# Kernel optimization log

Hardware: AMD Instinct MI355X
Metric: run time of the kernel (lower is better)

## Reference

```python
import jax, jax.numpy as jnp
import numpy as np

NUM_LAYERS = 5  # shared parameters across layers


def _crelu(z):
    # complex ReLU: ReLU applied independently to real and imag parts
    return jnp.maximum(z.real, 0.0) + 1j * jnp.maximum(z.imag, 0.0)


def _layer(Habs2, diagH, noise, maxpow, v, ar, dl, rc):
    # ---- u step ----
    # cov: [B,K,1] = |H|^2 @ |v|^2 (sum over last dim keepdim is identity for width-1) + noise
    cov = jnp.sum(Habs2 @ (jnp.abs(v) ** 2), axis=-1, keepdims=True) + noise[..., None]
    u = diagH[..., None] * v / cov  # [B,K,1] complex
    # ---- w step ---- (w_poly=None branch)
    err = 1.0 - jnp.conj(u) * diagH[..., None] * v
    w = 1.0 / err  # [B,K,1] complex
    # ---- v step ----
    v_tilde = jnp.conj(diagH)[..., None] * u * w  # [B,K,1]
    ul = (jnp.abs(u) ** 2) * jnp.abs(w)  # real [B,K,1]
    ul = jnp.sum(jnp.abs(jnp.swapaxes(Habs2, -2, -1) @ ul), axis=-1, keepdims=True)
    mu = jnp.maximum(jnp.abs(v_tilde) / jnp.sqrt(maxpow)[..., None] - ul, 0.0)
    ula = (ul + mu).astype(v_tilde.dtype)
    # ar + diagload branches: [B,K,1,1] @ [1,C] -> [B,K,1,C]
    vt = (v_tilde / ula)[..., None] @ ar + v_tilde[..., None] @ dl
    # nonlin + recombination: [B,K,1,C] @ [C,1] -> [B,K,1,1]
    vt = _crelu(vt) @ rc
    v_new = vt[..., 0]  # [B,K,1]
    # power correction
    cur = jnp.maximum(maxpow[..., None], jnp.abs(v_new) ** 2)
    corr = jnp.minimum(jnp.sqrt(maxpow[..., None] / cur), 1.0)
    return v_new * corr, u, w


def setup_inputs() -> dict:
    key = jax.random.key(0)
    ks = jax.random.split(key, 12)
    B, K, C = 64, 512, 4
    s = 1.0 / np.sqrt(C + 1)
    inp = {
        "h_re": jax.random.normal(ks[0], (B, K, K), jnp.float32),
        "h_im": jax.random.normal(ks[1], (B, K, K), jnp.float32),
        "user_noise_pow": jax.random.uniform(ks[2], (B, K), jnp.float32, 0.1, 1.0),
        "bss_maxpow": jnp.ones((B, K), jnp.float32),
        "v_in_re": jax.random.normal(ks[3], (B, K, 1), jnp.float32) * 0.5,
        "v_in_im": jax.random.normal(ks[4], (B, K, 1), jnp.float32) * 0.5,
        "ar_re": jax.random.normal(ks[5], (1, C), jnp.float32) * s,
        "ar_im": jax.random.normal(ks[6], (1, C), jnp.float32) * s,
        "dl_re": jax.random.normal(ks[7], (1, C), jnp.float32) * s,
        "dl_im": jax.random.normal(ks[8], (1, C), jnp.float32) * s,
        "rc_re": jax.random.normal(ks[9], (C, 1), jnp.float32) * s,
        "rc_im": jax.random.normal(ks[10], (C, 1), jnp.float32) * s,
    }
    return inp


def reference(h_re, h_im, user_noise_pow, bss_maxpow, v_in_re, v_in_im,
              ar_re, ar_im, dl_re, dl_im, rc_re, rc_im):
    H = (h_re + 1j * h_im).astype(jnp.complex64)
    Habs2 = h_re * h_re + h_im * h_im  # |H|^2, real [B,K,K]
    diagH = jnp.diagonal(H, axis1=-2, axis2=-1)  # [B,K]
    v = (v_in_re + 1j * v_in_im).astype(jnp.complex64)
    ar = (ar_re + 1j * ar_im).astype(jnp.complex64)
    dl = (dl_re + 1j * dl_im).astype(jnp.complex64)
    rc = (rc_re + 1j * rc_im).astype(jnp.complex64)
    vs = []
    for _ in range(NUM_LAYERS):
        v, u, w = _layer(Habs2, diagH, user_noise_pow, bss_maxpow, v, ar, dl, rc)
        vs.append(v)
    vstack = jnp.stack(vs, 0)  # [L,B,K,1] complex
    # return real/imag stacked so the output is a real tensor: [L,B,K,1,2]
    return jnp.stack([vstack.real, vstack.imag], axis=-1)
```

## Files before the change

kernel.cpp:

```cpp
#include <hip/hip_runtime.h>

#define B    64
#define K    512
#define C    4
#define NL   5
#define BK   (B*K)
#define ROWS 128
#define NT   1024
#define GRID (B*4)

typedef _Float16 half_t;
typedef _Float16 half8 __attribute__((ext_vector_type(8)));
typedef float    f4    __attribute__((ext_vector_type(4)));

#define HABS_BYTES (ROWS*K*2)
#define VST_OFF    (HABS_BYTES)
#define PART_OFF   (VST_OFF + K*8)
#define XSQ_OFF    (PART_OFF + 8*K*4)
#define DAB_OFF    (XSQ_OFF + K*4)
#define MPL_OFF    (DAB_OFF + ROWS*4)
#define NZ_OFF     (MPL_OFF + K*4)
#define SMEM_BYTES (NZ_OFF + ROWS*4)

__device__ __forceinline__ float ld_l3(const float* p) {
    return __uint_as_float(__hip_atomic_load((const unsigned*)p,
        __ATOMIC_RELAXED, __HIP_MEMORY_SCOPE_AGENT));
}
__device__ __forceinline__ void st_l3(float* p, float v) {
    __hip_atomic_store((unsigned*)p, __float_as_uint(v),
        __ATOMIC_RELAXED, __HIP_MEMORY_SCOPE_AGENT);
}
__device__ __forceinline__ void st_l3_2(float2* p, float2 v) {
    unsigned long long u = ((unsigned long long)__float_as_uint(v.y) << 32)
                         | (unsigned long long)__float_as_uint(v.x);
    __hip_atomic_store((unsigned long long*)p, u,
        __ATOMIC_RELAXED, __HIP_MEMORY_SCOPE_AGENT);
}
__device__ __forceinline__ float2 ld_l3_2(const float2* p) {
    unsigned long long u = __hip_atomic_load((const unsigned long long*)p,
        __ATOMIC_RELAXED, __HIP_MEMORY_SCOPE_AGENT);
    return make_float2(__uint_as_float((unsigned)(u & 0xffffffffu)),
                       __uint_as_float((unsigned)(u >> 32)));
}

__device__ __forceinline__ void quartet_barrier(unsigned* qb, unsigned target) {
    __syncthreads();
    if (threadIdx.x == 0) {
        __hip_atomic_fetch_add(qb, 1u, __ATOMIC_RELAXED,
                               __HIP_MEMORY_SCOPE_AGENT);
        while (__hip_atomic_load(qb, __ATOMIC_RELAXED,
                                 __HIP_MEMORY_SCOPE_AGENT) < target)
            __builtin_amdgcn_s_sleep(4);
    }
    __syncthreads();
}

__global__ __launch_bounds__(NT, 4) void k_all(
    const float* __restrict__ hre,  const float* __restrict__ him,
    const float* __restrict__ noise,const float* __restrict__ mp,
    const float* __restrict__ vre,  const float* __restrict__ vim,
    const float* __restrict__ ar_re,const float* __restrict__ ar_im,
    const float* __restrict__ dl_re,const float* __restrict__ dl_im,
    const float* __restrict__ rc_re,const float* __restrict__ rc_im,
    float2* __restrict__ vtilde,
    float*  __restrict__ ulpart,
    unsigned* __restrict__ bar,
    float* __restrict__ out)
{
    extern __shared__ char smem[];
    half_t* habs = (half_t*)smem;
    float2* vst  = (float2*)(smem + VST_OFF);
    float*  part = (float*) (smem + PART_OFF);
    float*  xsq  = (float*) (smem + XSQ_OFF);
    float*  dab  = (float*) (smem + DAB_OFF);
    float*  mpl  = (float*) (smem + MPL_OFF);
    float*  nz   = (float*) (smem + NZ_OFF);

    const int tid  = threadIdx.x;
    const int lane = tid & 63;
    const int w    = tid >> 6;
    const int b    = blockIdx.x & 63;
    const int q    = blockIdx.x >> 6;
    const int j0   = q * ROWS;
    unsigned* qb   = bar + ((unsigned)b << 5);

    {
        const size_t gb = ((size_t)b * K + j0) * K;
        const f4* rp = (const f4*)(hre + gb);
        const f4* ip = (const f4*)(him + gb);
        f4 lr0[2], lr1[2], li0[2], li1[2];
        lr0[0] = __builtin_nontemporal_load(rp + tid * 2);
        lr1[0] = __builtin_nontemporal_load(rp + tid * 2 + 1);
        li0[0] = __builtin_nontemporal_load(ip + tid * 2);
        li1[0] = __builtin_nontemporal_load(ip + tid * 2 + 1);
#pragma unroll
        for (int i = 0; i < 8; ++i) {
            const int cur = i & 1, nxt = cur ^ 1;
            if (i < 7) {
                const int e4 = (i + 1) * (NT * 2) + tid * 2;
                lr0[nxt] = __builtin_nontemporal_load(rp + e4);
                lr1[nxt] = __builtin_nontemporal_load(rp + e4 + 1);
                li0[nxt] = __builtin_nontemporal_load(ip + e4);
                li1[nxt] = __builtin_nontemporal_load(ip + e4 + 1);
            }
            const f4 r0 = lr0[cur], r1 = lr1[cur];
            const f4 m0 = li0[cur], m1 = li1[cur];
            float s[8];
            s[0] = r0.x*r0.x + m0.x*m0.x; s[1] = r0.y*r0.y + m0.y*m0.y;
            s[2] = r0.z*r0.z + m0.z*m0.z; s[3] = r0.w*r0.w + m0.w*m0.w;
            s[4] = r1.x*r1.x + m1.x*m1.x; s[5] = r1.y*r1.y + m1.y*m1.y;
            s[6] = r1.z*r1.z + m1.z*m1.z; s[7] = r1.w*r1.w + m1.w*m1.w;
            half8 hh;
#pragma unroll
            for (int t = 0; t < 8; ++t) hh[t] = (_Float16)s[t];
            const int e = i * (NT * 8) + tid * 8;
            *(half8*)(habs + e) = hh;
            const int row  = e >> 9;
            const int col0 = e & (K - 1);
            const int j    = j0 + row;
            if (j >= col0 && j < col0 + 8) dab[row] = s[j - col0];
        }
        if (tid < K) {
            float a = vre[b * K + tid], c = vim[b * K + tid];
            vst[tid] = make_float2(a, c);
            xsq[tid] = a * a + c * c;
            mpl[tid] = mp[b * K + tid];
        } else if (tid < K + ROWS) {
            nz[tid - K] = noise[b * K + j0 + (tid - K)];
        }
    }
    __syncthreads();

    for (int l = 0; l < NL; ++l) {
        const int buf = l & 1;
        const f4 xa = ((const f4*)xsq)[lane * 2];
        const f4 xb = ((const f4*)xsq)[lane * 2 + 1];
        half8 h[8];
        float rs[8];
#pragma unroll
        for (int r = 0; r < 8; ++r) {
            h[r] = *(const half8*)(habs + ((w * 8 + r) * K + lane * 8));
            float acc = (float)h[r][0]*xa.x + (float)h[r][1]*xa.y +
                        (float)h[r][2]*xa.z + (float)h[r][3]*xa.w +
                        (float)h[r][4]*xb.x + (float)h[r][5]*xb.y +
                        (float)h[r][6]*xb.z + (float)h[r][7]*xb.w;
#pragma unroll
            for (int off = 32; off; off >>= 1) acc += __shfl_xor(acc, off, 64);
            rs[r] = acc;
        }
        float ulv_own = 0.f;
        if (lane < 8) {
            const int row = w * 8 + lane;
            const int j   = j0 + row;
            const int bj  = b * K + j;
            float s = lane==0?rs[0]:lane==1?rs[1]:lane==2?rs[2]:lane==3?rs[3]:
                      lane==4?rs[4]:lane==5?rs[5]:lane==6?rs[6]:rs[7];
            const float cov = s + nz[row];
            const float d2  = dab[row];
            const float A   = d2 * xsq[j];
            const float ww  = cov / (cov - A);
            const float sc  = d2 * ww / cov;
            const float2 vv = vst[j];
            st_l3_2(&vtilde[buf * BK + bj], make_float2(sc * vv.x, sc * vv.y));
            ulv_own = A * ww / (cov * cov);
        }
        float ulv[8];
#pragma unroll
        for (int r = 0; r < 8; ++r) ulv[r] = __shfl(ulv_own, r, 64);

        float pw[8];
#pragma unroll
        for (int t = 0; t < 8; ++t) {
            pw[t] = (float)h[0][t]*ulv[0] + (float)h[1][t]*ulv[1] +
                    (float)h[2][t]*ulv[2] + (float)h[3][t]*ulv[3] +
                    (float)h[4][t]*ulv[4] + (float)h[5][t]*ulv[5] +
                    (float)h[6][t]*ulv[6] + (float)h[7][t]*ulv[7];
        }
        float* pr = part + (w & 7) * K + lane * 8;
        if (w < 8) {
#pragma unroll
            for (int t = 0; t < 8; ++t) pr[t] = pw[t];
        }
        __syncthreads();
        if (w >= 8) {
#pragma unroll
            for (int t = 0; t < 8; ++t) pr[t] += pw[t];
        }
        __syncthreads();
        float s2 = 0.f;
        if (tid < K) {
            s2 = part[tid]       + part[K + tid]   + part[2*K + tid] +
                 part[3*K + tid] + part[4*K + tid] + part[5*K + tid] +
                 part[6*K + tid] + part[7*K + tid];
            st_l3(&ulpart[(size_t)buf * (B*4*K) + ((size_t)(b*4 + q)) * K + tid],
                  s2);
        }
        quartet_barrier(qb, 4u * (unsigned)(l + 1));

        if (tid < K) {
            const int k  = tid;
            const int bk = b * K + k;
            const float* up = ulpart + (size_t)buf * (B*4*K) + (size_t)(b*4) * K;
            float ul = s2;
#pragma unroll
            for (int qq = 0; qq < 4; ++qq)
                if (qq != q) ul += ld_l3(up + qq * K + k);
            const float2 vt = ld_l3_2(&vtilde[buf * BK + bk]);
            const float p   = mpl[k];
            const float avt = sqrtf(vt.x*vt.x + vt.y*vt.y);
            const float mu  = fmaxf(avt / sqrtf(p) - ul, 0.f);
            const float inv = 1.f / (ul + mu);
            float ax = 0.f, ay = 0.f;
#pragma unroll
            for (int c = 0; c < C; ++c) {
                const float gre = ar_re[c] * inv + dl_re[c];
                const float gim = ar_im[c] * inv + dl_im[c];
                float zre = vt.x * gre - vt.y * gim;
                float zim = vt.x * gim + vt.y * gre;
                zre = fmaxf(zre, 0.f);
                zim = fmaxf(zim, 0.f);
                ax += zre * rc_re[c] - zim * rc_im[c];
                ay += zre * rc_im[c] + zim * rc_re[c];
            }
            const float n2   = ax*ax + ay*ay;
            const float cur  = fmaxf(p, n2);
            const float corr = fminf(sqrtf(p / cur), 1.f);
            ax *= corr; ay *= corr;
            if ((k >> 7) == q)
                ((float2*)out)[(size_t)l * BK + bk] = make_float2(ax, ay);
            vst[k] = make_float2(ax, ay);
            xsq[k] = ax * ax + ay * ay;
        }
        __syncthreads();
    }
}

extern "C" void kernel_launch(void* const* d_in, const int* in_sizes, int n_in,
                              void* d_out, int out_size, void* d_ws, size_t ws_size,
                              hipStream_t stream) {
    const float* hre   = (const float*)d_in[0];
    const float* him   = (const float*)d_in[1];
    const float* noise = (const float*)d_in[2];
    const float* mp    = (const float*)d_in[3];
    const float* vre   = (const float*)d_in[4];
    const float* vim   = (const float*)d_in[5];
    const float* ar_re = (const float*)d_in[6];
    const float* ar_im = (const float*)d_in[7];
    const float* dl_re = (const float*)d_in[8];
    const float* dl_im = (const float*)d_in[9];
    const float* rc_re = (const float*)d_in[10];
    const float* rc_im = (const float*)d_in[11];
    float* out = (float*)d_out;

    char*     ws     = (char*)d_ws;
    float2*   vtilde = (float2*)ws;
    float*    ulpart = (float*)(ws + 2*(size_t)BK*8);
    unsigned* bar    = (unsigned*)(ws + 2*(size_t)BK*8 + 2*(size_t)B*4*K*4);

    static bool attr_done = false;
    if (!attr_done) {
        hipFuncSetAttribute((const void*)k_all,
                            hipFuncAttributeMaxDynamicSharedMemorySize,
                            SMEM_BYTES);
        attr_done = true;
    }

    hipMemsetAsync(bar, 0, B * 32 * sizeof(unsigned), stream);

    hipLaunchKernelGGL(k_all, dim3(GRID), dim3(NT), SMEM_BYTES, stream,
                       hre, him, noise, mp, vre, vim,
                       ar_re, ar_im, dl_re, dl_im, rc_re, rc_im,
                       vtilde, ulpart, bar, out);
}
```

Measured before the change: 192.8 us.

## Keep |H|^2 tile in registers instead of shared memory across layers

The fp16 |H|^2 tile now stays in per-thread registers (8 half8 per thread) instead of a shared-memory buffer, and rows are interleaved across warps. The first layer's row sums are fused into the load loop. The partial-sum reduction now uses 16 shared slices with one barrier instead of two. The quartet barrier has every wave's lane 0 spin rather than using a trailing __syncthreads, and the vtilde load is hoisted. The aim is to remove LDS traffic and barriers, at the cost of higher register pressure and weaker memory-ordering guarantees on the spin wait.

```diff
diff --git a/kernel.cpp b/kernel.cpp
--- a/kernel.cpp
+++ b/kernel.cpp
@@ -13,14 +13,14 @@
 typedef _Float16 half8 __attribute__((ext_vector_type(8)));
 typedef float    f4    __attribute__((ext_vector_type(4)));
 
-#define HABS_BYTES (ROWS*K*2)
-#define VST_OFF    (HABS_BYTES)
-#define PART_OFF   (VST_OFF + K*8)
-#define XSQ_OFF    (PART_OFF + 8*K*4)
-#define DAB_OFF    (XSQ_OFF + K*4)
-#define MPL_OFF    (DAB_OFF + ROWS*4)
+#define PART_OFF   0
+#define VST_OFF    (36*K*4)
+#define XSQ_OFF    (VST_OFF + K*8)
+#define MPL_OFF    (XSQ_OFF + K*4)
 #define NZ_OFF     (MPL_OFF + K*4)
-#define SMEM_BYTES (NZ_OFF + ROWS*4)
+#define DAB_OFF    (NZ_OFF + ROWS*4)
+#define RSB_OFF    (DAB_OFF + ROWS*4)
+#define SMEM_BYTES (RSB_OFF + ROWS*4)
 
 __device__ __forceinline__ float ld_l3(const float* p) {
     return __uint_as_float(__hip_atomic_load((const unsigned*)p,
@@ -41,18 +41,6 @@
         __ATOMIC_RELAXED, __HIP_MEMORY_SCOPE_AGENT);
     return make_float2(__uint_as_float((unsigned)(u & 0xffffffffu)),
                        __uint_as_float((unsigned)(u >> 32)));
-}
-
-__device__ __forceinline__ void quartet_barrier(unsigned* qb, unsigned target) {
-    __syncthreads();
-    if (threadIdx.x == 0) {
-        __hip_atomic_fetch_add(qb, 1u, __ATOMIC_RELAXED,
-                               __HIP_MEMORY_SCOPE_AGENT);
-        while (__hip_atomic_load(qb, __ATOMIC_RELAXED,
-                                 __HIP_MEMORY_SCOPE_AGENT) < target)
-            __builtin_amdgcn_s_sleep(4);
-    }
-    __syncthreads();
 }
 
 __global__ __launch_bounds__(NT, 4) void k_all(
@@ -68,13 +56,13 @@
     float* __restrict__ out)
 {
     extern __shared__ char smem[];
-    half_t* habs = (half_t*)smem;
-    float2* vst  = (float2*)(smem + VST_OFF);
-    float*  part = (float*) (smem + PART_OFF);
-    float*  xsq  = (float*) (smem + XSQ_OFF);
-    float*  dab  = (float*) (smem + DAB_OFF);
-    float*  mpl  = (float*) (smem + MPL_OFF);
-    float*  nz   = (float*) (smem + NZ_OFF);
+    float*  part  = (float*) (smem + PART_OFF);
+    float2* vst   = (float2*)(smem + VST_OFF);
+    float*  xsq   = (float*) (smem + XSQ_OFF);
+    float*  mpl   = (float*) (smem + MPL_OFF);
+    float*  nz    = (float*) (smem + NZ_OFF);
+    float*  dab   = (float*) (smem + DAB_OFF);
+    float*  rsbuf = (float*) (smem + RSB_OFF);
 
     const int tid  = threadIdx.x;
     const int lane = tid & 63;
@@ -84,7 +72,20 @@
     const int j0   = q * ROWS;
     unsigned* qb   = bar + ((unsigned)b << 5);
 
+    if (tid < K) {
+        float a = vre[b * K + tid], c2 = vim[b * K + tid];
+        vst[tid] = make_float2(a, c2);
+        xsq[tid] = a * a + c2 * c2;
+        mpl[tid] = mp[b * K + tid];
+    } else if (tid < K + ROWS) {
+        nz[tid - K] = noise[b * K + j0 + (tid - K)];
+    }
+    __syncthreads();
+
+    half8 h[8];
     {
+        const f4 xa = ((const f4*)xsq)[lane * 2];
+        const f4 xb = ((const f4*)xsq)[lane * 2 + 1];
         const size_t gb = ((size_t)b * K + j0) * K;
         const f4* rp = (const f4*)(hre + gb);
         const f4* ip = (const f4*)(him + gb);
@@ -113,49 +114,41 @@
             half8 hh;
 #pragma unroll
             for (int t = 0; t < 8; ++t) hh[t] = (_Float16)s[t];
-            const int e = i * (NT * 8) + tid * 8;
-            *(half8*)(habs + e) = hh;
-            const int row  = e >> 9;
-            const int col0 = e & (K - 1);
+            h[i] = hh;
+            const int row  = i * 16 + w;
+            const int col0 = lane * 8;
             const int j    = j0 + row;
             if (j >= col0 && j < col0 + 8) dab[row] = s[j - col0];
-        }
-        if (tid < K) {
-            float a = vre[b * K + tid], c = vim[b * K + tid];
-            vst[tid] = make_float2(a, c);
-            xsq[tid] = a * a + c * c;
-            mpl[tid] = mp[b * K + tid];
-        } else if (tid < K + ROWS) {
-            nz[tid - K] = noise[b * K + j0 + (tid - K)];
-        }
-    }
-    __syncthreads();
+            float acc = s[0]*xa.x + s[1]*xa.y + s[2]*xa.z + s[3]*xa.w +
+                        s[4]*xb.x + s[5]*xb.y + s[6]*xb.z + s[7]*xb.w;
+#pragma unroll
+            for (int off = 32; off; off >>= 1) acc += __shfl_xor(acc, off, 64);
+            if (lane == 0) rsbuf[row] = acc;
+        }
+    }
 
     for (int l = 0; l < NL; ++l) {
         const int buf = l & 1;
-        const f4 xa = ((const f4*)xsq)[lane * 2];
-        const f4 xb = ((const f4*)xsq)[lane * 2 + 1];
-        half8 h[8];
-        float rs[8];
-#pragma unroll
-        for (int r = 0; r < 8; ++r) {
-            h[r] = *(const half8*)(habs + ((w * 8 + r) * K + lane * 8));
-            float acc = (float)h[r][0]*xa.x + (float)h[r][1]*xa.y +
-                        (float)h[r][2]*xa.z + (float)h[r][3]*xa.w +
-                        (float)h[r][4]*xb.x + (float)h[r][5]*xb.y +
-                        (float)h[r][6]*xb.z + (float)h[r][7]*xb.w;
-#pragma unroll
-            for (int off = 32; off; off >>= 1) acc += __shfl_xor(acc, off, 64);
-            rs[r] = acc;
+        if (l > 0) {
+            const f4 xa = ((const f4*)xsq)[lane * 2];
+            const f4 xb = ((const f4*)xsq)[lane * 2 + 1];
+#pragma unroll
+            for (int r = 0; r < 8; ++r) {
+                float acc = (float)h[r][0]*xa.x + (float)h[r][1]*xa.y +
+                            (float)h[r][2]*xa.z + (float)h[r][3]*xa.w +
+                            (float)h[r][4]*xb.x + (float)h[r][5]*xb.y +
+                            (float)h[r][6]*xb.z + (float)h[r][7]*xb.w;
+#pragma unroll
+                for (int off = 32; off; off >>= 1) acc += __shfl_xor(acc, off, 64);
+                if (lane == 0) rsbuf[r * 16 + w] = acc;
+            }
         }
         float ulv_own = 0.f;
         if (lane < 8) {
-            const int row = w * 8 + lane;
+            const int row = 16 * lane + w;
             const int j   = j0 + row;
             const int bj  = b * K + j;
-            float s = lane==0?rs[0]:lane==1?rs[1]:lane==2?rs[2]:lane==3?rs[3]:
-                      lane==4?rs[4]:lane==5?rs[5]:lane==6?rs[6]:rs[7];
-            const float cov = s + nz[row];
+            const float cov = rsbuf[row] + nz[row];
             const float d2  = dab[row];
             const float A   = d2 * xsq[j];
             const float ww  = cov / (cov - A);
@@ -176,36 +169,39 @@
                     (float)h[4][t]*ulv[4] + (float)h[5][t]*ulv[5] +
                     (float)h[6][t]*ulv[6] + (float)h[7][t]*ulv[7];
         }
-        float* pr = part + (w & 7) * K + lane * 8;
-        if (w < 8) {
-#pragma unroll
-            for (int t = 0; t < 8; ++t) pr[t] = pw[t];
-        }
+        float* pr = part + w * K + lane * 8;
+#pragma unroll
+        for (int t = 0; t < 8; ++t) pr[t] = pw[t];
         __syncthreads();
-        if (w >= 8) {
-#pragma unroll
-            for (int t = 0; t < 8; ++t) pr[t] += pw[t];
-        }
-        __syncthreads();
+
         float s2 = 0.f;
         if (tid < K) {
-            s2 = part[tid]       + part[K + tid]   + part[2*K + tid] +
-                 part[3*K + tid] + part[4*K + tid] + part[5*K + tid] +
-                 part[6*K + tid] + part[7*K + tid];
+#pragma unroll
+            for (int ws2 = 0; ws2 < 16; ++ws2) s2 += part[ws2 * K + tid];
             st_l3(&ulpart[(size_t)buf * (B*4*K) + ((size_t)(b*4 + q)) * K + tid],
                   s2);
         }
-        quartet_barrier(qb, 4u * (unsigned)(l + 1));
+        __syncthreads();
+        if (tid == 0)
+            __hip_atomic_fetch_add(qb, 1u, __ATOMIC_RELAXED,
+                                   __HIP_MEMORY_SCOPE_AGENT);
+        if (lane == 0) {
+            const unsigned target = 4u * (unsigned)(l + 1);
+            while (__hip_atomic_load(qb, __ATOMIC_RELAXED,
+                                     __HIP_MEMORY_SCOPE_AGENT) < target)
+                __builtin_amdgcn_s_sleep(2);
+        }
+        asm volatile("" ::: "memory");
 
         if (tid < K) {
             const int k  = tid;
             const int bk = b * K + k;
             const float* up = ulpart + (size_t)buf * (B*4*K) + (size_t)(b*4) * K;
+            const float2 vt = ld_l3_2(&vtilde[buf * BK + bk]);
             float ul = s2;
 #pragma unroll
             for (int qq = 0; qq < 4; ++qq)
                 if (qq != q) ul += ld_l3(up + qq * K + k);
-            const float2 vt = ld_l3_2(&vtilde[buf * BK + bk]);
             const float p   = mpl[k];
             const float avt = sqrtf(vt.x*vt.x + vt.y*vt.y);
             const float mu  = fmaxf(avt / sqrtf(p) - ul, 0.f);
```

Result: faster. 188.6 us (-2.1%).
